# Optimization experiments

Hardware: AMD Instinct MI355X
Metric: run time of the kernel (lower is better)

## Reference

```python
import jax, jax.numpy as jnp
import numpy as np

KH, KW = 3, 3  # window_size[1], window_size[2]
SH, SW = 1, 1  # strides
FILTERS = 64


def _extract_patches(x, kh, kw, sh, sw):
    # TF tf.image.extract_patches ordering: depth = (row, col, channel), channel fastest.
    B, H, W, C = x.shape
    Ho = (H - kh) // sh + 1
    Wo = (W - kw) // sw + 1
    # stack kh*kw shifted views -> (B, Ho, Wo, kh*kw, C)
    views = [x[:, i:i + (Ho - 1) * sh + 1:sh, j:j + (Wo - 1) * sw + 1:sw, :]
             for i in range(kh) for j in range(kw)]
    patches = jnp.stack(views, axis=3)
    return patches.reshape(B, Ho, Wo, kh * kw * C)


def setup_inputs() -> dict:
    key = jax.random.key(0)
    k1, k2 = jax.random.split(key)
    B, H, W, C = 8, 32, 32, 32
    K = KH * KW * C  # 288
    x = jax.random.normal(k1, (B, H, W, C), dtype=jnp.float32)
    w = jax.random.normal(k2, (1, 1, 1, K, FILTERS), dtype=jnp.float32) * 0.05
    bias = jnp.zeros((FILTERS,), dtype=jnp.float32)
    return {"x": x, "w": w, "bias": bias}


def reference(x, w, bias):
    # patches: (B, Ho, Wo, K)
    patches = _extract_patches(x, KH, KW, SH, SW)
    # broadcast add: (B, Ho, Wo, K, F)
    s = patches[..., None] + w
    # tropical max-plus minus min-plus over the patch axis, plus bias
    return jnp.max(s, axis=3) - jnp.min(s, axis=3) + bias
```

## Files before the change

kernel.cpp:

```cpp
#include <hip/hip_runtime.h>
#include <math.h>


#define TPB 256
#define PIX 4

__device__ __forceinline__ float fmax3(float a, float b, float c) {
    return fmaxf(fmaxf(a, b), c);
}
__device__ __forceinline__ float fmin3(float a, float b, float c) {
    return fminf(fminf(a, b), c);
}

__global__ __launch_bounds__(TPB) void trop_kernel(
    const float* __restrict__ x,
    const float* __restrict__ w,
    const float* __restrict__ bias,
    float* __restrict__ out)
{
    extern __shared__ float wlds[];

    const int tid  = threadIdx.x;
    const int lane = tid & 63;
    const int wv   = tid >> 6;

    const int pix0 = blockIdx.x * (4 * PIX) + wv * PIX;

    {
        const float4* src = (const float4*)w;
        float4* dst = (float4*)wlds;
#pragma unroll
        for (int i = 0; i < 18; ++i) dst[tid + i * 256] = src[tid + i * 256];
    }

    int xoffp[PIX];
#pragma unroll
    for (int p = 0; p < PIX; ++p) {
        const int pid = pix0 + p;
        const int wo = pid % 30;
        const int t  = pid / 30;
        const int ho = t % 30;
        const int b  = t / 30;
        xoffp[p] = __builtin_amdgcn_readfirstlane((((b * 32 + ho) * 32) + wo) * 32);
    }

    float amax[PIX], amin[PIX];
#pragma unroll
    for (int p = 0; p < PIX; ++p) { amax[p] = -INFINITY; amin[p] = INFINITY; }

    __syncthreads();

#pragma unroll
    for (int tap = 0; tap < 9; ++tap) {
        const int dy = tap / 3;
        const int dx = tap % 3;
        const int xoff = (dy * 32 + dx) * 32;
        const float* wl = wlds + tap * 2048;
#pragma unroll
        for (int c = 0; c < 32; c += 4) {
            const float w0 = wl[(c + 0) * 64 + lane];
            const float w1 = wl[(c + 1) * 64 + lane];
            const float w2 = wl[(c + 2) * 64 + lane];
            const float w3 = wl[(c + 3) * 64 + lane];
#pragma unroll
            for (int p = 0; p < PIX; ++p) {
                const float* xb = x + xoffp[p] + xoff;
                const float s0 = xb[c + 0] + w0;
                const float s1 = xb[c + 1] + w1;
                const float s2 = xb[c + 2] + w2;
                const float s3 = xb[c + 3] + w3;
                amax[p] = fmax3(amax[p], fmax3(s0, s1, s2), s3);
                amin[p] = fmin3(amin[p], fmin3(s0, s1, s2), s3);
            }
        }
    }

    const float bv = bias[lane];
#pragma unroll
    for (int p = 0; p < PIX; ++p)
        out[(pix0 + p) * 64 + lane] = amax[p] - amin[p] + bv;
}

extern "C" void kernel_launch(void* const* d_in, const int* in_sizes, int n_in,
                              void* d_out, int out_size, void* d_ws, size_t ws_size,
                              hipStream_t stream) {
    const float* x    = (const float*)d_in[0];
    const float* w    = (const float*)d_in[1];
    const float* bias = (const float*)d_in[2];
    float* out = (float*)d_out;

    static int attr_done = 0;
    if (!attr_done) {
        (void)hipFuncSetAttribute((const void*)trop_kernel,
                                  hipFuncAttributeMaxDynamicSharedMemorySize,
                                  73728);
        attr_done = 1;
    }

    trop_kernel<<<dim3(450), dim3(TPB), 73728, stream>>>(x, w, bias, out);
}
```

Measured before the change: 73.78 us.

## Split reduction axis across waves with register-resident weights and LDS combine

Each of the four waves in a block now takes a 72-element slice of the 288-long patch axis and keeps its weight slice in registers, rather than every block copying the full 72 KB weight tensor into LDS. Each block handles 8 pixels, with partial max and min values combined through a small shared array after one barrier. The launch grows to 900 blocks and uses float4 x loads, with a 4-blocks-per-CU launch bound. This removes the per-block weight staging and the large LDS footprint that limited occupancy, at the cost of higher register pressure and an extra cross-wave reduction.

```diff
diff --git a/kernel.cpp b/kernel.cpp
--- a/kernel.cpp
+++ b/kernel.cpp
@@ -3,7 +3,8 @@
 
 
 #define TPB 256
-#define PIX 4
+#define CPB 8
+#define KPW 72
 
 __device__ __forceinline__ float fmax3(float a, float b, float c) {
     return fmaxf(fmaxf(a, b), c);
@@ -12,73 +13,84 @@
     return fminf(fminf(a, b), c);
 }
 
-__global__ __launch_bounds__(TPB) void trop_kernel(
+__global__ __launch_bounds__(TPB, 4) void trop_kernel(
     const float* __restrict__ x,
     const float* __restrict__ w,
     const float* __restrict__ bias,
     float* __restrict__ out)
 {
-    extern __shared__ float wlds[];
+    __shared__ float2 part[4][CPB][64];
 
     const int tid  = threadIdx.x;
     const int lane = tid & 63;
     const int wv   = tid >> 6;
+    const int K0   = __builtin_amdgcn_readfirstlane(wv * KPW);
 
-    const int pix0 = blockIdx.x * (4 * PIX) + wv * PIX;
+    const int pix0 = blockIdx.x * CPB;
 
-    {
-        const float4* src = (const float4*)w;
-        float4* dst = (float4*)wlds;
+    float4 wr[18];
 #pragma unroll
-        for (int i = 0; i < 18; ++i) dst[tid + i * 256] = src[tid + i * 256];
+    for (int j = 0; j < 18; ++j) {
+        const int k = K0 + 4 * j;
+        wr[j].x = w[(k + 0) * 64 + lane];
+        wr[j].y = w[(k + 1) * 64 + lane];
+        wr[j].z = w[(k + 2) * 64 + lane];
+        wr[j].w = w[(k + 3) * 64 + lane];
     }
 
-    int xoffp[PIX];
+    int pbase[CPB];
 #pragma unroll
-    for (int p = 0; p < PIX; ++p) {
+    for (int p = 0; p < CPB; ++p) {
         const int pid = pix0 + p;
         const int wo = pid % 30;
         const int t  = pid / 30;
         const int ho = t % 30;
         const int b  = t / 30;
-        xoffp[p] = __builtin_amdgcn_readfirstlane((((b * 32 + ho) * 32) + wo) * 32);
+        pbase[p] = __builtin_amdgcn_readfirstlane((((b * 32 + ho) * 32) + wo) * 32);
     }
 
-    float amax[PIX], amin[PIX];
+    float amax[CPB], amin[CPB];
 #pragma unroll
-    for (int p = 0; p < PIX; ++p) { amax[p] = -INFINITY; amin[p] = INFINITY; }
+    for (int p = 0; p < CPB; ++p) { amax[p] = -INFINITY; amin[p] = INFINITY; }
+
+#pragma unroll
+    for (int j = 0; j < 18; ++j) {
+        const int k   = K0 + 4 * j;
+        const int tap = k >> 5;
+        const int c   = k & 31;
+        const int dy  = tap / 3;
+        const int dx  = tap - dy * 3;
+        const int xoff = __builtin_amdgcn_readfirstlane((dy * 32 + dx) * 32 + c);
+#pragma unroll
+        for (int p = 0; p < CPB; ++p) {
+            const float4 xv = *(const float4*)(x + pbase[p] + xoff);
+            const float s0 = xv.x + wr[j].x;
+            const float s1 = xv.y + wr[j].y;
+            const float s2 = xv.z + wr[j].z;
+            const float s3 = xv.w + wr[j].w;
+            amax[p] = fmax3(amax[p], fmax3(s0, s1, s2), s3);
+            amin[p] = fmin3(amin[p], fmin3(s0, s1, s2), s3);
+        }
+    }
+
+#pragma unroll
+    for (int p = 0; p < CPB; ++p)
+        part[wv][p][lane] = make_float2(amax[p], amin[p]);
 
     __syncthreads();
 
-#pragma unroll
-    for (int tap = 0; tap < 9; ++tap) {
-        const int dy = tap / 3;
-        const int dx = tap % 3;
-        const int xoff = (dy * 32 + dx) * 32;
-        const float* wl = wlds + tap * 2048;
-#pragma unroll
-        for (int c = 0; c < 32; c += 4) {
-            const float w0 = wl[(c + 0) * 64 + lane];
-            const float w1 = wl[(c + 1) * 64 + lane];
-            const float w2 = wl[(c + 2) * 64 + lane];
-            const float w3 = wl[(c + 3) * 64 + lane];
-#pragma unroll
-            for (int p = 0; p < PIX; ++p) {
-                const float* xb = x + xoffp[p] + xoff;
-                const float s0 = xb[c + 0] + w0;
-                const float s1 = xb[c + 1] + w1;
-                const float s2 = xb[c + 2] + w2;
-                const float s3 = xb[c + 3] + w3;
-                amax[p] = fmax3(amax[p], fmax3(s0, s1, s2), s3);
-                amin[p] = fmin3(amin[p], fmin3(s0, s1, s2), s3);
-            }
-        }
-    }
-
     const float bv = bias[lane];
 #pragma unroll
-    for (int p = 0; p < PIX; ++p)
-        out[(pix0 + p) * 64 + lane] = amax[p] - amin[p] + bv;
+    for (int i = 0; i < 2; ++i) {
+        const int p = 2 * wv + i;
+        const float2 a = part[0][p][lane];
+        const float2 b = part[1][p][lane];
+        const float2 c = part[2][p][lane];
+        const float2 d = part[3][p][lane];
+        const float m = fmaxf(fmaxf(a.x, b.x), fmaxf(c.x, d.x));
+        const float n = fminf(fminf(a.y, b.y), fminf(c.y, d.y));
+        out[(pix0 + p) * 64 + lane] = m - n + bv;
+    }
 }
 
 extern "C" void kernel_launch(void* const* d_in, const int* in_sizes, int n_in,
@@ -89,13 +101,5 @@
     const float* bias = (const float*)d_in[2];
     float* out = (float*)d_out;
 
-    static int attr_done = 0;
-    if (!attr_done) {
-        (void)hipFuncSetAttribute((const void*)trop_kernel,
-                                  hipFuncAttributeMaxDynamicSharedMemorySize,
-                                  73728);
-        attr_done = 1;
-    }
-
-    trop_kernel<<<dim3(450), dim3(TPB), 73728, stream>>>(x, w, bias, out);
+    trop_kernel<<<dim3(900), dim3(TPB), 0, stream>>>(x, w, bias, out);
 }
```

Result: slower. 75.49 us (+2.3%).
